# Kernel tuning notes

Measured on AMD Instinct MI355X. Metric: run time of the kernel, lower is better.

Reference implementation:

```python
import jax, jax.numpy as jnp
import numpy as np

B, T, D = 2, 1024, 2048
H, HKV, DH = 16, 4, 128
G = H // HKV  # GQA groups
F = 5632
ROPE_THETA = 10000.0
EPS = 1e-6


def _rope_tables(t, dh, theta):
    inv = 1.0 / (theta ** (np.arange(0, dh, 2, dtype=np.float32) / dh))  # [dh//2]
    ang = np.outer(np.arange(t, dtype=np.float32), inv)                  # [T, dh//2]
    return jnp.asarray(np.cos(ang)), jnp.asarray(np.sin(ang))


def setup_inputs() -> dict:
    key = jax.random.key(0)
    ks = jax.random.split(key, 9)
    s = 0.02
    cos, sin = _rope_tables(T, DH, ROPE_THETA)
    return {
        "x": jax.random.normal(ks[0], (B, T, D), jnp.float32),
        "freqs_cos": cos,
        "freqs_sin": sin,
        "w_norm1": jnp.ones((D,), jnp.float32),
        "w_norm2": jnp.ones((D,), jnp.float32),
        "wq": jax.random.normal(ks[1], (D, H * DH), jnp.float32) * s,
        "wk": jax.random.normal(ks[2], (D, HKV * DH), jnp.float32) * s,
        "wv": jax.random.normal(ks[3], (D, HKV * DH), jnp.float32) * s,
        "wo": jax.random.normal(ks[4], (D, D), jnp.float32) * s,
        "w1": jax.random.normal(ks[5], (D, F), jnp.float32) * s,
        "w2": jax.random.normal(ks[6], (F, D), jnp.float32) * s,
        "w3": jax.random.normal(ks[7], (D, F), jnp.float32) * s,
    }


def _rmsnorm(x, w):
    var = jnp.mean(jnp.square(x), axis=-1, keepdims=True)
    return x * jax.lax.rsqrt(var + EPS) * w


def _apply_rope(x, cos, sin):
    # x: [B, T, nH, DH]; cos/sin: [T, DH//2]
    xr = x.reshape(*x.shape[:-1], DH // 2, 2)
    x0, x1 = xr[..., 0], xr[..., 1]
    c = cos[None, :, None, :]
    s = sin[None, :, None, :]
    o0 = x0 * c - x1 * s
    o1 = x0 * s + x1 * c
    return jnp.stack([o0, o1], axis=-1).reshape(x.shape)


def reference(x, freqs_cos, freqs_sin, w_norm1, w_norm2, wq, wk, wv, wo, w1, w2, w3):
    residual = x
    xn = _rmsnorm(x, w_norm1)
    q = (xn @ wq).reshape(B, T, H, DH)
    k = (xn @ wk).reshape(B, T, HKV, DH)
    v = (xn @ wv).reshape(B, T, HKV, DH)
    q = _apply_rope(q, freqs_cos, freqs_sin)
    k = _apply_rope(k, freqs_cos, freqs_sin)
    # grouped heads: q -> [B, HKV, G, T, DH]; k,v -> [B, HKV, T, DH]
    q = q.transpose(0, 2, 1, 3).reshape(B, HKV, G, T, DH)
    k = k.transpose(0, 2, 1, 3)
    v = v.transpose(0, 2, 1, 3)
    scale = DH ** -0.5
    scores = jnp.einsum("bkgtd,bksd->bkgts", q, k) * scale  # [B,HKV,G,T,T]
    causal = jnp.tril(jnp.ones((T, T), dtype=bool))
    scores = jnp.where(causal, scores, -jnp.inf)
    attn = jax.nn.softmax(scores, axis=-1)
    out = jnp.einsum("bkgts,bksd->bkgtd", attn, v)  # [B,HKV,G,T,DH]
    out = out.reshape(B, H, T, DH).transpose(0, 2, 1, 3).reshape(B, T, D)
    x = residual + out @ wo
    h = _rmsnorm(x, w_norm2)
    ffn = (jax.nn.silu(h @ w1) * (h @ w3)) @ w2
    return x + ffn
```

## Files before the change

kernel.cpp:

```cpp
#include <hip/hip_runtime.h>
#include <hip/hip_bf16.h>
#include <math.h>

typedef __hip_bfloat16 bf16;
typedef __attribute__((ext_vector_type(8))) short bf16x8;
typedef __attribute__((ext_vector_type(4))) float f32x4;

__device__ __forceinline__ float b2f(bf16 v) { return __bfloat162float(v); }
__device__ __forceinline__ bf16  f2b(float v) { return __float2bfloat16(v); }

constexpr int Bc = 2, Tc = 1024, Dc = 2048, Hc = 16, HKVc = 4, DHc = 128, Fc = 5632;
constexpr int Mr = Bc * Tc;
constexpr int Nqkv = Hc * DHc + 2 * HKVc * DHc;

__device__ __forceinline__ void g2l16(void* lds, const void* g) {
  __builtin_amdgcn_global_load_lds(
      (const __attribute__((address_space(1))) unsigned int*)g,
      (__attribute__((address_space(3))) unsigned int*)lds, 16, 0, 0);
}

__global__ __launch_bounds__(256) void tcast_k(const float* __restrict__ src,
                                               bf16* __restrict__ dst,
                                               int N, int K) {
  __shared__ bf16 tile[64][68];
  const int t = threadIdx.x;
  const int n0 = blockIdx.x * 64, k0 = blockIdx.y * 64;
#pragma unroll
  for (int it = 0; it < 4; ++it) {
    const int kl = it * 16 + (t >> 4);
    const int nl = (t & 15) * 4;
    float4 v = *reinterpret_cast<const float4*>(src + (size_t)(k0 + kl) * N + n0 + nl);
    tile[kl][nl]     = f2b(v.x);
    tile[kl][nl + 1] = f2b(v.y);
    tile[kl][nl + 2] = f2b(v.z);
    tile[kl][nl + 3] = f2b(v.w);
  }
  __syncthreads();
  union { uint4 u; bf16 h[8]; } o;
#pragma unroll
  for (int it = 0; it < 2; ++it) {
    const int nl = it * 32 + (t >> 3);
    const int kl = (t & 7) * 8;
#pragma unroll
    for (int j = 0; j < 8; ++j) o.h[j] = tile[kl + j][nl];
    *reinterpret_cast<uint4*>(dst + (size_t)(n0 + nl) * K + k0 + kl) = o.u;
  }
}

__global__ __launch_bounds__(256) void tcast_ffn(const float* __restrict__ src,
                                                 bf16* __restrict__ dst,
                                                 int off) {
  __shared__ bf16 tile[64][68];
  const int t = threadIdx.x;
  const int n0 = blockIdx.x * 64, k0 = blockIdx.y * 64;
#pragma unroll
  for (int it = 0; it < 4; ++it) {
    const int kl = it * 16 + (t >> 4);
    const int nl = (t & 15) * 4;
    float4 v = *reinterpret_cast<const float4*>(src + (size_t)(k0 + kl) * Fc + n0 + nl);
    tile[kl][nl]     = f2b(v.x);
    tile[kl][nl + 1] = f2b(v.y);
    tile[kl][nl + 2] = f2b(v.z);
    tile[kl][nl + 3] = f2b(v.w);
  }
  __syncthreads();
  union { uint4 u; bf16 h[8]; } o;
#pragma unroll
  for (int it = 0; it < 2; ++it) {
    const int nl = it * 32 + (t >> 3);
    const int kl = (t & 7) * 8;
#pragma unroll
    for (int j = 0; j < 8; ++j) o.h[j] = tile[kl + j][nl];
    const int n = n0 + nl;
    const int r = ((n >> 4) << 5) + (n & 15) + off;
    *reinterpret_cast<uint4*>(dst + (size_t)r * Dc + k0 + kl) = o.u;
  }
}

__global__ __launch_bounds__(256) void rmsnorm_k(const float* __restrict__ x,
                                                 const float* __restrict__ w,
                                                 bf16* __restrict__ out) {
  const size_t rbase = (size_t)blockIdx.x * Dc;
  float ss = 0.f;
  for (int i = threadIdx.x; i < Dc; i += 256) {
    float v = x[rbase + i];
    ss += v * v;
  }
#pragma unroll
  for (int off = 32; off > 0; off >>= 1) ss += __shfl_down(ss, off, 64);
  __shared__ float red[4];
  const int lane = threadIdx.x & 63, wid = threadIdx.x >> 6;
  if (lane == 0) red[wid] = ss;
  __syncthreads();
  const float scale = rsqrtf((red[0] + red[1] + red[2] + red[3]) / (float)Dc + 1e-6f);
  for (int i = threadIdx.x; i < Dc; i += 256)
    out[rbase + i] = f2b(x[rbase + i] * scale * w[i]);
}

__global__ __launch_bounds__(256) void reduce4_rms(const float* __restrict__ P,
                                                   const float* __restrict__ x,
                                                   const float* __restrict__ w,
                                                   float* __restrict__ xat,
                                                   bf16* __restrict__ hb) {
  constexpr size_t PS = (size_t)Mr * Dc;
  const size_t base4 = (size_t)blockIdx.x * (Dc / 4);
  const int t = threadIdx.x;
  float4 v[2];
  float ss = 0.f;
#pragma unroll
  for (int j = 0; j < 2; ++j) {
    const size_t c4 = base4 + t + j * 256;
    float4 a = reinterpret_cast<const float4*>(x)[c4];
#pragma unroll
    for (int z = 0; z < 4; ++z) {
      float4 q = reinterpret_cast<const float4*>(P + z * PS)[c4];
      a.x += q.x; a.y += q.y; a.z += q.z; a.w += q.w;
    }
    reinterpret_cast<float4*>(xat)[c4] = a;
    ss += a.x * a.x + a.y * a.y + a.z * a.z + a.w * a.w;
    v[j] = a;
  }
#pragma unroll
  for (int off = 32; off > 0; off >>= 1) ss += __shfl_down(ss, off, 64);
  __shared__ float red[4];
  const int lane = t & 63, wid = t >> 6;
  if (lane == 0) red[wid] = ss;
  __syncthreads();
  const float scale = rsqrtf((red[0] + red[1] + red[2] + red[3]) / (float)Dc + 1e-6f);
  bf16* hrow = hb + (size_t)blockIdx.x * Dc;
#pragma unroll
  for (int j = 0; j < 2; ++j) {
    const int c = (t + j * 256) * 4;
    hrow[c]     = f2b(v[j].x * scale * w[c]);
    hrow[c + 1] = f2b(v[j].y * scale * w[c + 1]);
    hrow[c + 2] = f2b(v[j].z * scale * w[c + 2]);
    hrow[c + 3] = f2b(v[j].w * scale * w[c + 3]);
  }
}

__global__ __launch_bounds__(256) void reduce4_add(const float* __restrict__ P,
                                                   const float* __restrict__ res,
                                                   float* __restrict__ out) {
  constexpr size_t PS = (size_t)Mr * Dc;
  const size_t c4 = (size_t)blockIdx.x * 256 + threadIdx.x;
  float4 a = reinterpret_cast<const float4*>(res)[c4];
#pragma unroll
  for (int z = 0; z < 4; ++z) {
    float4 q = reinterpret_cast<const float4*>(P + z * PS)[c4];
    a.x += q.x; a.y += q.y; a.z += q.z; a.w += q.w;
  }
  reinterpret_cast<float4*>(out)[c4] = a;
}

template <bool ADDRES>
__global__ __launch_bounds__(256) void gemm128(const bf16* __restrict__ A,
                                               const bf16* __restrict__ Bt,
                                               const float* __restrict__ Res,
                                               void* __restrict__ Out,
                                               int N, int K) {
  __shared__ __align__(16) bf16 As[128 * 32];
  __shared__ __align__(16) bf16 Bs[128 * 32];
  const int t = threadIdx.x;
  const int bm = blockIdx.y * 128, bn = blockIdx.x * 128;
  const int lane = t & 63, wv = t >> 6;
  const int wm = (wv & 1) * 64, wn = (wv >> 1) * 64;
  const int sr = t >> 2, sc = (t & 3) * 8;
  const bf16* ga = A + (size_t)(bm + sr) * K + sc;
  const bf16* gb = Bt + (size_t)(bn + sr) * K + sc;
  bf16* lA0 = As + sr * 32 + sc;
  bf16* lA1 = As + (64 + sr) * 32 + sc;
  bf16* lB0 = Bs + sr * 32 + sc;
  bf16* lB1 = Bs + (64 + sr) * 32 + sc;
  const size_t rstep = (size_t)64 * K;
  f32x4 acc[4][4] = {};
  const int fr = lane & 15, fko = (lane >> 4) * 8;
  for (int k0 = 0; k0 < K; k0 += 32) {
    __syncthreads();
    g2l16(lA0, ga + k0);
    g2l16(lA1, ga + rstep + k0);
    g2l16(lB0, gb + k0);
    g2l16(lB1, gb + rstep + k0);
    __syncthreads();
    bf16x8 af[4], bff[4];
#pragma unroll
    for (int i = 0; i < 4; ++i)
      af[i] = *reinterpret_cast<const bf16x8*>(As + (wm + i * 16 + fr) * 32 + fko);
#pragma unroll
    for (int j = 0; j < 4; ++j)
      bff[j] = *reinterpret_cast<const bf16x8*>(Bs + (wn + j * 16 + fr) * 32 + fko);
#pragma unroll
    for (int i = 0; i < 4; ++i)
#pragma unroll
      for (int j = 0; j < 4; ++j)
        acc[i][j] = __builtin_amdgcn_mfma_f32_16x16x32_bf16(af[i], bff[j], acc[i][j], 0, 0, 0);
  }
  const int er = (lane >> 4) * 4, ec = lane & 15;
#pragma unroll
  for (int i = 0; i < 4; ++i)
#pragma unroll
    for (int j = 0; j < 4; ++j) {
      const int row = bm + wm + i * 16 + er;
      const int col = bn + wn + j * 16 + ec;
#pragma unroll
      for (int r = 0; r < 4; ++r) {
        const size_t idx = (size_t)(row + r) * N + col;
        if (ADDRES) ((float*)Out)[idx] = Res[idx] + acc[i][j][r];
        else        ((bf16*)Out)[idx] = f2b(acc[i][j][r]);
      }
    }
}

template <int K>
__global__ __launch_bounds__(512, 2) void ffn_gemm256(const bf16* __restrict__ A,
                                                      const bf16* __restrict__ B,
                                                      bf16* __restrict__ act) {
  constexpr int NT = K / 64;
  constexpr int NIT = NT / 2;
  __shared__ bf16 As[2 * 256 * 64];
  __shared__ bf16 Bs[3 * 256 * 64];
  const int tid = threadIdx.x;
  const int lane = tid & 63, wv = tid >> 6;
  const int wr = wv >> 2, wc = wv & 3;
  const int fr = lane & 15, quad = lane >> 4;
  const int swz = fr & 7;
  const int bm = blockIdx.y * 256;
  const int bn = blockIdx.x * 256;
  const int lrow = tid >> 3;
  const int scol = ((tid & 7) ^ (lrow & 7)) * 8;
  const size_t rstep = (size_t)64 * K;

  auto stageA = [&](int t, int half) {
    const int buf = (t & 1) * 16384;
    const bf16* g = A + (size_t)(bm + half * 128 + lrow) * K + t * 64 + scol;
    bf16* d = As + buf + half * 8192 + (size_t)tid * 8;
    g2l16(d, g);
    g2l16(d + 4096, g + rstep);
  };
  auto stageB = [&](int t, int half, int buf) {
    const bf16* g = B + (size_t)(bn + half * 128 + lrow) * K + t * 64 + scol;
    bf16* d = Bs + buf * 16384 + half * 8192 + (size_t)tid * 8;
    g2l16(d, g);
    g2l16(d + 4096, g + rstep);
  };

  f32x4 acc[8][4] = {};
  const int u0 = (quad ^ swz) * 8;

  stageA(0, 0); stageA(0, 1);
  stageB(0, 0, 0); stageB(0, 1, 0);
  stageB(1, 0, 1); stageB(1, 1, 1);
  asm volatile("s_waitcnt vmcnt(4)" ::: "memory");
  __builtin_amdgcn_s_barrier();

  int rb0 = 0, rb1 = 1, sb = 2;
  for (int it = 0; it < NIT; ++it) {
    const int t1 = 2 * it + 1;
#pragma unroll
    for (int j = 0; j < 8; ++j) {
      const int bufT = (j < 4) ? 0 : 16384;
      const int bufB = ((j < 4) ? rb0 : rb1) * 16384;
      const int qr4 = ((j & 3) >> 1) * 4, qc2 = ((j & 3) & 1) * 2;
      bf16x8 af[4][2], bv[2][2];
      const bf16* Ab = As + bufT + (size_t)(wr * 128 + fr) * 64;
      const bf16* Bb = Bs + bufB + (size_t)(wc * 64 + fr) * 64;
#pragma unroll
      for (int ii = 0; ii < 4; ++ii) {
        af[ii][0] = *reinterpret_cast<const bf16x8*>(Ab + (qr4 + ii) * 1024 + u0);
        af[ii][1] = *reinterpret_cast<const bf16x8*>(Ab + (qr4 + ii) * 1024 + (u0 ^ 32));
      }
#pragma unroll
      for (int jj = 0; jj < 2; ++jj) {
        bv[jj][0] = *reinterpret_cast<const bf16x8*>(Bb + (qc2 + jj) * 1024 + u0);
        bv[jj][1] = *reinterpret_cast<const bf16x8*>(Bb + (qc2 + jj) * 1024 + (u0 ^ 32));
      }
      if (j == 0)      stageA(t1, 0);
      else if (j == 1) stageA(t1, 1);
      else if (j == 2) { if (2 * it + 2 < NT) stageB(2 * it + 2, 0, sb); }
      else if (j == 3) { if (2 * it + 2 < NT) stageB(2 * it + 2, 1, sb); }
      else if (j == 4) { if (2 * it + 2 < NT) stageA(2 * it + 2, 0); }
      else if (j == 5) { if (2 * it + 2 < NT) stageA(2 * it + 2, 1); }
      else if (j == 6) { if (2 * it + 3 < NT) stageB(2 * it + 3, 0, rb0); }
      else             { if (2 * it + 3 < NT) stageB(2 * it + 3, 1, rb0); }
      __builtin_amdgcn_s_barrier();
      asm volatile("s_waitcnt lgkmcnt(0)" ::: "memory");
      __builtin_amdgcn_sched_barrier(0);
      __builtin_amdgcn_s_setprio(1);
#pragma unroll
      for (int ii = 0; ii < 4; ++ii)
#pragma unroll
        for (int jj = 0; jj < 2; ++jj) {
          acc[qr4 + ii][qc2 + jj] = __builtin_amdgcn_mfma_f32_16x16x32_bf16(
              af[ii][0], bv[jj][0], acc[qr4 + ii][qc2 + jj], 0, 0, 0);
          acc[qr4 + ii][qc2 + jj] = __builtin_amdgcn_mfma_f32_16x16x32_bf16(
              af[ii][1], bv[jj][1], acc[qr4 + ii][qc2 + jj], 0, 0, 0);
        }
      __builtin_amdgcn_s_setprio(0);
      if (j == 3) {
        if (2 * it + 2 < NT) asm volatile("s_waitcnt vmcnt(4)" ::: "memory");
        else                 asm volatile("s_waitcnt vmcnt(0)" ::: "memory");
      } else if (j == 7) {
        if (2 * it + 3 < NT)      asm volatile("s_waitcnt vmcnt(4)" ::: "memory");
        else if (2 * it + 2 < NT) asm volatile("s_waitcnt vmcnt(0)" ::: "memory");
      }
      __builtin_amdgcn_s_barrier();
    }
    const int nrb0 = sb; sb = rb1; rb1 = rb0; rb0 = nrb0;
  }

  const int er = quad * 4, ec = lane & 15;
#pragma unroll
  for (int i = 0; i < 8; ++i) {
    const int row = bm + wr * 128 + i * 16 + er;
#pragma unroll
    for (int jp = 0; jp < 2; ++jp) {
      const f32x4 g = acc[i][2 * jp], u = acc[i][2 * jp + 1];
      const int f = blockIdx.x * 128 + wc * 32 + jp * 16 + ec;
#pragma unroll
      for (int r = 0; r < 4; ++r) {
        const float sg = g[r] / (1.f + __expf(-g[r]));
        act[(size_t)(row + r) * Fc + f] = f2b(sg * u[r]);
      }
    }
  }
}

template <int KFULL, int KSUB>
__global__ __launch_bounds__(512, 2) void gemm256sk(const bf16* __restrict__ A,
                                                    const bf16* __restrict__ Bt,
                                                    float* __restrict__ Part,
                                                    int N) {
  constexpr int NT = KSUB / 64;
  constexpr int NIT = NT / 2;
  __shared__ bf16 As[2 * 256 * 64];
  __shared__ bf16 Bs[3 * 256 * 64];
  const int tid = threadIdx.x;
  const int lane = tid & 63, wv = tid >> 6;
  const int wr = wv >> 2, wc = wv & 3;
  const int fr = lane & 15, quad = lane >> 4;
  const int swz = fr & 7;
  const int bm = blockIdx.y * 256;
  const int bn = blockIdx.x * 256;
  const int kbase = blockIdx.z * KSUB;
  const int lrow = tid >> 3;
  const int scol = ((tid & 7) ^ (lrow & 7)) * 8;
  const size_t rstep = (size_t)64 * KFULL;

  auto stageA = [&](int t, int half) {
    const int buf = (t & 1) * 16384;
    const bf16* g = A + (size_t)(bm + half * 128 + lrow) * KFULL + kbase + t * 64 + scol;
    bf16* d = As + buf + half * 8192 + (size_t)tid * 8;
    g2l16(d, g);
    g2l16(d + 4096, g + rstep);
  };
  auto stageB = [&](int t, int half, int buf) {
    const bf16* g = Bt + (size_t)(bn + half * 128 + lrow) * KFULL + kbase + t * 64 + scol;
    bf16* d = Bs + buf * 16384 + half * 8192 + (size_t)tid * 8;
    g2l16(d, g);
    g2l16(d + 4096, g + rstep);
  };

  f32x4 acc[8][4] = {};
  const int u0 = (quad ^ swz) * 8;

  stageA(0, 0); stageA(0, 1);
  stageB(0, 0, 0); stageB(0, 1, 0);
  stageB(1, 0, 1); stageB(1, 1, 1);
  asm volatile("s_waitcnt vmcnt(4)" ::: "memory");
  __builtin_amdgcn_s_barrier();

  int rb0 = 0, rb1 = 1, sb = 2;
  for (int it = 0; it < NIT; ++it) {
    const int t1 = 2 * it + 1;
#pragma unroll
    for (int j = 0; j < 8; ++j) {
      const int bufT = (j < 4) ? 0 : 16384;
      const int bufB = ((j < 4) ? rb0 : rb1) * 16384;
      const int qr4 = ((j & 3) >> 1) * 4, qc2 = ((j & 3) & 1) * 2;
      bf16x8 af[4][2], bv[2][2];
      const bf16* Ab = As + bufT + (size_t)(wr * 128 + fr) * 64;
      const bf16* Bb = Bs + bufB + (size_t)(wc * 64 + fr) * 64;
#pragma unroll
      for (int ii = 0; ii < 4; ++ii) {
        af[ii][0] = *reinterpret_cast<const bf16x8*>(Ab + (qr4 + ii) * 1024 + u0);
        af[ii][1] = *reinterpret_cast<const bf16x8*>(Ab + (qr4 + ii) * 1024 + (u0 ^ 32));
      }
#pragma unroll
      for (int jj = 0; jj < 2; ++jj) {
        bv[jj][0] = *reinterpret_cast<const bf16x8*>(Bb + (qc2 + jj) * 1024 + u0);
        bv[jj][1] = *reinterpret_cast<const bf16x8*>(Bb + (qc2 + jj) * 1024 + (u0 ^ 32));
      }
      if (j == 0)      stageA(t1, 0);
      else if (j == 1) stageA(t1, 1);
      else if (j == 2) { if (2 * it + 2 < NT) stageB(2 * it + 2, 0, sb); }
      else if (j == 3) { if (2 * it + 2 < NT) stageB(2 * it + 2, 1, sb); }
      else if (j == 4) { if (2 * it + 2 < NT) stageA(2 * it + 2, 0); }
      else if (j == 5) { if (2 * it + 2 < NT) stageA(2 * it + 2, 1); }
      else if (j == 6) { if (2 * it + 3 < NT) stageB(2 * it + 3, 0, rb0); }
      else             { if (2 * it + 3 < NT) stageB(2 * it + 3, 1, rb0); }
      __builtin_amdgcn_s_barrier();
      asm volatile("s_waitcnt lgkmcnt(0)" ::: "memory");
      __builtin_amdgcn_sched_barrier(0);
      __builtin_amdgcn_s_setprio(1);
#pragma unroll
      for (int ii = 0; ii < 4; ++ii)
#pragma unroll
        for (int jj = 0; jj < 2; ++jj) {
          acc[qr4 + ii][qc2 + jj] = __builtin_amdgcn_mfma_f32_16x16x32_bf16(
              af[ii][0], bv[jj][0], acc[qr4 + ii][qc2 + jj], 0, 0, 0);
          acc[qr4 + ii][qc2 + jj] = __builtin_amdgcn_mfma_f32_16x16x32_bf16(
              af[ii][1], bv[jj][1], acc[qr4 + ii][qc2 + jj], 0, 0, 0);
        }
      __builtin_amdgcn_s_setprio(0);
      if (j == 3) {
        if (2 * it + 2 < NT) asm volatile("s_waitcnt vmcnt(4)" ::: "memory");
        else                 asm volatile("s_waitcnt vmcnt(0)" ::: "memory");
      } else if (j == 7) {
        if (2 * it + 3 < NT)      asm volatile("s_waitcnt vmcnt(4)" ::: "memory");
        else if (2 * it + 2 < NT) asm volatile("s_waitcnt vmcnt(0)" ::: "memory");
      }
      __builtin_amdgcn_s_barrier();
    }
    const int nrb0 = sb; sb = rb1; rb1 = rb0; rb0 = nrb0;
  }

  float* P = Part + (size_t)blockIdx.z * ((size_t)Mr * N);
  const int er = quad * 4, ec = lane & 15;
#pragma unroll
  for (int i = 0; i < 8; ++i) {
    const int row = bm + wr * 128 + i * 16 + er;
#pragma unroll
    for (int jc = 0; jc < 4; ++jc) {
      const int col = bn + wc * 64 + jc * 16 + ec;
#pragma unroll
      for (int r = 0; r < 4; ++r)
        P[(size_t)(row + r) * N + col] = acc[i][jc][r];
    }
  }
}

__global__ __launch_bounds__(256) void repack_k(const bf16* __restrict__ qkv,
                                                const float* __restrict__ cosb,
                                                const float* __restrict__ sinb,
                                                bf16* __restrict__ Qr,
                                                bf16* __restrict__ Kr,
                                                bf16* __restrict__ Vt) {
  const int bt = blockIdx.x;
  const int b = bt >> 10, tp = bt & (Tc - 1);
  const int t0 = threadIdx.x;
  const bf16* row = qkv + (size_t)bt * Nqkv;
#pragma unroll
  for (int k = 0; k < 4; ++k) {
    int p2 = k * 256 + t0;
    int hh = p2 >> 6, i = p2 & 63;
    float c = cosb[tp * 64 + i], sn = sinb[tp * 64 + i];
    float x0 = b2f(row[hh * 128 + 2 * i]), x1 = b2f(row[hh * 128 + 2 * i + 1]);
    bf16* dst = Qr + ((size_t)(b * Hc + hh) * Tc + tp) * DHc + 2 * i;
    dst[0] = f2b(x0 * c - x1 * sn);
    dst[1] = f2b(x0 * sn + x1 * c);
  }
  {
    int hh = t0 >> 6, i = t0 & 63;
    float c = cosb[tp * 64 + i], sn = sinb[tp * 64 + i];
    float x0 = b2f(row[2048 + hh * 128 + 2 * i]), x1 = b2f(row[2048 + hh * 128 + 2 * i + 1]);
    bf16* dst = Kr + ((size_t)(b * HKVc + hh) * Tc + tp) * DHc + 2 * i;
    dst[0] = f2b(x0 * c - x1 * sn);
    dst[1] = f2b(x0 * sn + x1 * c);
  }
#pragma unroll
  for (int k = 0; k < 2; ++k) {
    int e = k * 256 + t0;
    int kvh = e >> 7, dd = e & 127;
    Vt[((size_t)(b * HKVc + kvh) * DHc + dd) * Tc + tp] = row[2560 + e];
  }
}

__global__ __launch_bounds__(256) void fattn(const bf16* __restrict__ Qr,
                                             const bf16* __restrict__ Kr,
                                             const bf16* __restrict__ Vt,
                                             bf16* __restrict__ ao) {
  __shared__ __align__(16) bf16 Ks[64 * 136];
  __shared__ __align__(16) bf16 Vts[128 * 72];
  __shared__ __align__(16) bf16 Ps[4][16 * 72];
  const int idx = blockIdx.x;
  const int r = idx & 15;
  const int qt = (r & 1) ? (15 - (r >> 1)) : (r >> 1);
  const int h = (idx >> 4) & 15;
  const int b = idx >> 8;
  const int kv = h >> 2;
  const int t = threadIdx.x, lane = t & 63, wv = t >> 6;
  const int fr = lane & 15, quad = lane >> 4;

  const bf16* Qbase = Qr + ((size_t)(b * Hc + h) * Tc + qt * 64) * DHc;
  const bf16* Kbase = Kr + (size_t)(b * HKVc + kv) * Tc * DHc;
  const bf16* Vbase = Vt + (size_t)(b * HKVc + kv) * DHc * Tc;

  bf16x8 qf[4];
#pragma unroll
  for (int c = 0; c < 4; ++c)
    qf[c] = *reinterpret_cast<const bf16x8*>(Qbase + (size_t)(wv * 16 + fr) * DHc + c * 32 + quad * 8);

  float m[4], l[4];
  f32x4 o[8] = {};
#pragma unroll
  for (int r2 = 0; r2 < 4; ++r2) { m[r2] = -3.0e38f; l[r2] = 0.f; }

  for (int kt = 0; kt <= qt; ++kt) {
    __syncthreads();
    {
      const bf16* src = Kbase + (size_t)kt * 64 * DHc;
#pragma unroll
      for (int i2 = 0; i2 < 4; ++i2) {
        int flat = i2 * 256 + t;
        int row = flat >> 4, c16 = flat & 15;
        uint4 v = *reinterpret_cast<const uint4*>(src + (size_t)row * DHc + c16 * 8);
        *reinterpret_cast<uint4*>(&Ks[row * 136 + c16 * 8]) = v;
      }
#pragma unroll
      for (int i2 = 0; i2 < 4; ++i2) {
        int flat = i2 * 256 + t;
        int row = flat >> 3, c8 = flat & 7;
        uint4 v = *reinterpret_cast<const uint4*>(Vbase + (size_t)row * Tc + kt * 64 + c8 * 8);
        *reinterpret_cast<uint4*>(&Vts[row * 72 + c8 * 8]) = v;
      }
    }
    __syncthreads();
    f32x4 s[4];
#pragma unroll
    for (int cb = 0; cb < 4; ++cb) {
      f32x4 acc = {};
#pragma unroll
      for (int kc = 0; kc < 4; ++kc) {
        bf16x8 kf = *reinterpret_cast<const bf16x8*>(&Ks[(cb * 16 + fr) * 136 + kc * 32 + quad * 8]);
        acc = __builtin_amdgcn_mfma_f32_16x16x32_bf16(qf[kc], kf, acc, 0, 0, 0);
      }
      s[cb] = acc * 0.08838834764831845f;
    }
    if (kt == qt) {
#pragma unroll
      for (int cb = 0; cb < 4; ++cb)
#pragma unroll
        for (int r2 = 0; r2 < 4; ++r2) {
          int key = cb * 16 + fr;
          int qg = wv * 16 + quad * 4 + r2;
          if (key > qg) s[cb][r2] = -3.0e38f;
        }
    }
    float tm[4], ts[4];
#pragma unroll
    for (int r2 = 0; r2 < 4; ++r2)
      tm[r2] = fmaxf(fmaxf(s[0][r2], s[1][r2]), fmaxf(s[2][r2], s[3][r2]));
#pragma unroll
    for (int off = 1; off < 16; off <<= 1)
#pragma unroll
      for (int r2 = 0; r2 < 4; ++r2)
        tm[r2] = fmaxf(tm[r2], __shfl_xor(tm[r2], off, 64));
    float al[4];
#pragma unroll
    for (int r2 = 0; r2 < 4; ++r2) {
      float mn = fmaxf(m[r2], tm[r2]);
      al[r2] = __expf(m[r2] - mn);
      m[r2] = mn;
      ts[r2] = 0.f;
    }
#pragma unroll
    for (int cb = 0; cb < 4; ++cb)
#pragma unroll
      for (int r2 = 0; r2 < 4; ++r2) {
        float e = __expf(s[cb][r2] - m[r2]);
        s[cb][r2] = e;
        ts[r2] += e;
      }
#pragma unroll
    for (int off = 1; off < 16; off <<= 1)
#pragma unroll
      for (int r2 = 0; r2 < 4; ++r2)
        ts[r2] += __shfl_xor(ts[r2], off, 64);
#pragma unroll
    for (int r2 = 0; r2 < 4; ++r2) l[r2] = l[r2] * al[r2] + ts[r2];
#pragma unroll
    for (int db = 0; db < 8; ++db)
#pragma unroll
      for (int r2 = 0; r2 < 4; ++r2) o[db][r2] *= al[r2];
    bf16* pw = Ps[wv];
#pragma unroll
    for (int cb = 0; cb < 4; ++cb)
#pragma unroll
      for (int r2 = 0; r2 < 4; ++r2)
        pw[(quad * 4 + r2) * 72 + cb * 16 + fr] = f2b(s[cb][r2]);
    bf16x8 pa[2];
    pa[0] = *reinterpret_cast<const bf16x8*>(&pw[fr * 72 + quad * 8]);
    pa[1] = *reinterpret_cast<const bf16x8*>(&pw[fr * 72 + 32 + quad * 8]);
#pragma unroll
    for (int db = 0; db < 8; ++db) {
      bf16x8 v0 = *reinterpret_cast<const bf16x8*>(&Vts[(db * 16 + fr) * 72 + quad * 8]);
      bf16x8 v1 = *reinterpret_cast<const bf16x8*>(&Vts[(db * 16 + fr) * 72 + 32 + quad * 8]);
      o[db] = __builtin_amdgcn_mfma_f32_16x16x32_bf16(pa[0], v0, o[db], 0, 0, 0);
      o[db] = __builtin_amdgcn_mfma_f32_16x16x32_bf16(pa[1], v1, o[db], 0, 0, 0);
    }
  }
#pragma unroll
  for (int r2 = 0; r2 < 4; ++r2) {
    float inv = 1.f / l[r2];
    int qg = qt * 64 + wv * 16 + quad * 4 + r2;
    bf16* orow = ao + (size_t)(b * Tc + qg) * Dc + h * DHc;
#pragma unroll
    for (int db = 0; db < 8; ++db)
      orow[db * 16 + fr] = f2b(o[db][r2] * inv);
  }
}

extern "C" void kernel_launch(void* const* d_in, const int* in_sizes, int n_in,
                              void* d_out, int out_size, void* d_ws, size_t ws_size,
                              hipStream_t stream) {
  const float* x    = (const float*)d_in[0];
  const float* fcos = (const float*)d_in[1];
  const float* fsin = (const float*)d_in[2];
  const float* wn1  = (const float*)d_in[3];
  const float* wn2  = (const float*)d_in[4];
  const float* wq   = (const float*)d_in[5];
  const float* wk   = (const float*)d_in[6];
  const float* wv   = (const float*)d_in[7];
  const float* wo   = (const float*)d_in[8];
  const float* w1   = (const float*)d_in[9];
  const float* w2   = (const float*)d_in[10];
  const float* w3   = (const float*)d_in[11];

  char* p = (char*)d_ws;
  bf16* wqkv_t = (bf16*)p;                 p += (size_t)Nqkv * Dc * 2;
  bf16* qkv    = (bf16*)p;                 p += (size_t)Mr * Nqkv * 2;
  float* xat   = (float*)d_ws;
  bf16* wo_t = (bf16*)p;                   p += (size_t)Dc * Dc * 2;
  bf16* w13t = (bf16*)p;                   p += (size_t)2 * Fc * Dc * 2;
  bf16* w2t  = w13t;
  bf16* xn   = (bf16*)p;                   p += (size_t)Mr * Dc * 2;
  bf16* ao   = (bf16*)p;                   p += (size_t)Mr * Dc * 2;
  bf16* act  = (bf16*)p;                   p += (size_t)Mr * Fc * 2;
  float* Pbuf = (float*)p;                 p += (size_t)4 * Mr * Dc * 4;
  bf16* hb = xn;
  bf16* Qr = act;
  bf16* Kr = act + (size_t)Mr * Hc * DHc;
  bf16* Vtb = Kr + (size_t)Mr * HKVc * DHc;

  const dim3 blk(256);
  tcast_k<<<dim3(32, 32), blk, 0, stream>>>(wq, wqkv_t, 2048, 2048);
  tcast_k<<<dim3(8, 32), blk, 0, stream>>>(wk, wqkv_t + (size_t)2048 * 2048, 512, 2048);
  tcast_k<<<dim3(8, 32), blk, 0, stream>>>(wv, wqkv_t + (size_t)2560 * 2048, 512, 2048);
  tcast_k<<<dim3(32, 32), blk, 0, stream>>>(wo, wo_t, 2048, 2048);
  tcast_ffn<<<dim3(88, 32), blk, 0, stream>>>(w1, w13t, 0);
  tcast_ffn<<<dim3(88, 32), blk, 0, stream>>>(w3, w13t, 16);

  rmsnorm_k<<<Mr, blk, 0, stream>>>(x, wn1, xn);
  gemm128<false><<<dim3(Nqkv / 128, Mr / 128), blk, 0, stream>>>(xn, wqkv_t, nullptr, qkv, Nqkv, Dc);
  repack_k<<<Mr, blk, 0, stream>>>(qkv, fcos, fsin, Qr, Kr, Vtb);
  fattn<<<Bc * Hc * 16, blk, 0, stream>>>(Qr, Kr, Vtb, ao);
  gemm256sk<Dc, 512><<<dim3(Dc / 256, Mr / 256, 4), dim3(512), 0, stream>>>(ao, wo_t, Pbuf, Dc);
  reduce4_rms<<<Mr, blk, 0, stream>>>(Pbuf, x, wn2, xat, hb);
  ffn_gemm256<Dc><<<dim3(2 * Fc / 256, Mr / 256), dim3(512), 0, stream>>>(hb, w13t, act);
  tcast_k<<<dim3(32, 88), blk, 0, stream>>>(w2, w2t, 2048, 5632);
  gemm256sk<Fc, 1408><<<dim3(Dc / 256, Mr / 256, 4), dim3(512), 0, stream>>>(act, w2t, Pbuf, Dc);
  reduce4_add<<<Mr * Dc / 1024, blk, 0, stream>>>(Pbuf, xat, (float*)d_out);
}
```

Baseline: 571.8 us.

## Read K and V fragments directly from global memory in attention, drop LDS staging

The flash-attention kernel no longer stages K and V^T tiles into shared memory with block-wide barriers. Each wave now loads its MFMA operand fragments straight from global memory, relying on L2 and cache reuse across the four waves. It also raises wave priority around the MFMA loops with s_setprio. This removes the two __syncthreads per tile and the LDS traffic, but each wave re-fetches the same K/V data with less coalesced 16-byte loads, so latency is more exposed.

```diff
diff --git a/kernel.cpp b/kernel.cpp
--- a/kernel.cpp
+++ b/kernel.cpp
@@ -478,8 +478,6 @@
                                              const bf16* __restrict__ Kr,
                                              const bf16* __restrict__ Vt,
                                              bf16* __restrict__ ao) {
-  __shared__ __align__(16) bf16 Ks[64 * 136];
-  __shared__ __align__(16) bf16 Vts[128 * 72];
   __shared__ __align__(16) bf16 Ps[4][16 * 72];
   const int idx = blockIdx.x;
   const int r = idx & 15;
@@ -505,36 +503,21 @@
   for (int r2 = 0; r2 < 4; ++r2) { m[r2] = -3.0e38f; l[r2] = 0.f; }
 
   for (int kt = 0; kt <= qt; ++kt) {
-    __syncthreads();
-    {
-      const bf16* src = Kbase + (size_t)kt * 64 * DHc;
-#pragma unroll
-      for (int i2 = 0; i2 < 4; ++i2) {
-        int flat = i2 * 256 + t;
-        int row = flat >> 4, c16 = flat & 15;
-        uint4 v = *reinterpret_cast<const uint4*>(src + (size_t)row * DHc + c16 * 8);
-        *reinterpret_cast<uint4*>(&Ks[row * 136 + c16 * 8]) = v;
-      }
-#pragma unroll
-      for (int i2 = 0; i2 < 4; ++i2) {
-        int flat = i2 * 256 + t;
-        int row = flat >> 3, c8 = flat & 7;
-        uint4 v = *reinterpret_cast<const uint4*>(Vbase + (size_t)row * Tc + kt * 64 + c8 * 8);
-        *reinterpret_cast<uint4*>(&Vts[row * 72 + c8 * 8]) = v;
-      }
-    }
-    __syncthreads();
+    const bf16* Kt = Kbase + (size_t)kt * 64 * DHc;
+    const bf16* Vtt = Vbase + kt * 64;
     f32x4 s[4];
+    __builtin_amdgcn_s_setprio(1);
 #pragma unroll
     for (int cb = 0; cb < 4; ++cb) {
       f32x4 acc = {};
 #pragma unroll
       for (int kc = 0; kc < 4; ++kc) {
-        bf16x8 kf = *reinterpret_cast<const bf16x8*>(&Ks[(cb * 16 + fr) * 136 + kc * 32 + quad * 8]);
+        bf16x8 kf = *reinterpret_cast<const bf16x8*>(Kt + (size_t)(cb * 16 + fr) * DHc + kc * 32 + quad * 8);
         acc = __builtin_amdgcn_mfma_f32_16x16x32_bf16(qf[kc], kf, acc, 0, 0, 0);
       }
       s[cb] = acc * 0.08838834764831845f;
     }
+    __builtin_amdgcn_s_setprio(0);
     if (kt == qt) {
 #pragma unroll
       for (int cb = 0; cb < 4; ++cb)
@@ -590,13 +573,15 @@
     bf16x8 pa[2];
     pa[0] = *reinterpret_cast<const bf16x8*>(&pw[fr * 72 + quad * 8]);
     pa[1] = *reinterpret_cast<const bf16x8*>(&pw[fr * 72 + 32 + quad * 8]);
+    __builtin_amdgcn_s_setprio(1);
 #pragma unroll
     for (int db = 0; db < 8; ++db) {
-      bf16x8 v0 = *reinterpret_cast<const bf16x8*>(&Vts[(db * 16 + fr) * 72 + quad * 8]);
-      bf16x8 v1 = *reinterpret_cast<const bf16x8*>(&Vts[(db * 16 + fr) * 72 + 32 + quad * 8]);
+      bf16x8 v0 = *reinterpret_cast<const bf16x8*>(Vtt + (size_t)(db * 16 + fr) * Tc + quad * 8);
+      bf16x8 v1 = *reinterpret_cast<const bf16x8*>(Vtt + (size_t)(db * 16 + fr) * Tc + 32 + quad * 8);
       o[db] = __builtin_amdgcn_mfma_f32_16x16x32_bf16(pa[0], v0, o[db], 0, 0, 0);
       o[db] = __builtin_amdgcn_mfma_f32_16x16x32_bf16(pa[1], v1, o[db], 0, 0, 0);
     }
+    __builtin_amdgcn_s_setprio(0);
   }
 #pragma unroll
   for (int r2 = 0; r2 < 4; ++r2) {
```

Measured after the change: 650.1 us. 13.7% more time.
